# Performance work log

Measured on AMD Instinct MI355X. Metric: run time of the kernel, lower is better.

## Reference

```python
import jax, jax.numpy as jnp
import numpy as np

N = 10000      # nodes
E = 320000     # edges
IN = 256       # in_dim == out_dim
H = 8          # heads
D = 32         # head_dim = in_dim // heads
CLAMP = 5.0
BN_EPS = 1e-5


def setup_inputs() -> dict:
    key = jax.random.key(0)
    ks = jax.random.split(key, 24)
    s = 0.05
    nrm = lambda k, shape, sc=s: (jax.random.normal(k, shape, jnp.float32) * sc)
    inp = {
        "x": nrm(ks[0], (N, IN), 1.0),
        "edge_attr": nrm(ks[1], (E, IN), 1.0),
        "log_deg": jax.random.uniform(ks[2], (N, 1), jnp.float32, 0.1, 3.0),
        "edge_index": jax.random.randint(ks[3], (2, E), 0, N, jnp.int32),
        # attention projections (stored [in, out]; x @ W + b)
        "Qw": nrm(ks[4], (IN, H * D)), "Qb": jnp.zeros((H * D,), jnp.float32),
        "Kw": nrm(ks[5], (IN, H * D)), "Kb": jnp.zeros((H * D,), jnp.float32),
        "Ew": nrm(ks[6], (IN, H * D * 2)), "Eb": jnp.zeros((H * D * 2,), jnp.float32),
        "Vw": nrm(ks[7], (IN, H * D)), "Vb": jnp.zeros((H * D,), jnp.float32),
        "Aw": nrm(ks[8], (D, H, 1)),
        "VeRow": nrm(ks[9], (D, H, D)),
        # layer params
        "deg_coef": nrm(ks[10], (1, H * D, 2)),
        "Now": nrm(ks[11], (H * D, IN)), "Nob": jnp.zeros((IN,), jnp.float32),
        "Eow": nrm(ks[12], (H * D, IN)), "Eob": jnp.zeros((IN,), jnp.float32),
        "bn1n_g": jnp.ones((IN,), jnp.float32), "bn1n_b": jnp.zeros((IN,), jnp.float32),
        "bn1e_g": jnp.ones((IN,), jnp.float32), "bn1e_b": jnp.zeros((IN,), jnp.float32),
        "f1w": nrm(ks[13], (IN, 2 * IN)), "f1b": jnp.zeros((2 * IN,), jnp.float32),
        "f2w": nrm(ks[14], (2 * IN, IN)), "f2b": jnp.zeros((IN,), jnp.float32),
        "bn2_g": jnp.ones((IN,), jnp.float32), "bn2_b": jnp.zeros((IN,), jnp.float32),
    }
    return inp


def _bn(x, g, b):
    # batch_norm with batch statistics (bn_no_runner=True => track_running_stats=False)
    mu = jnp.mean(x, axis=0)
    var = jnp.mean(jnp.square(x - mu), axis=0)  # biased, as torch BN
    return (x - mu) * jax.lax.rsqrt(var + BN_EPS) * g + b


def _attention(x, edge_attr, edge_index, Qw, Qb, Kw, Kb, Ew, Eb, Vw, Vb, Aw, VeRow):
    n = x.shape[0]
    src, dst = edge_index[0], edge_index[1]
    Qh = (x @ Qw + Qb).reshape(n, H, D)
    Kh = (x @ Kw + Kb).reshape(n, H, D)
    Vh = (x @ Vw + Vb).reshape(n, H, D)
    Ex = (edge_attr @ Ew + Eb).reshape(-1, H, 2 * D)
    score1 = Kh[src] + Qh[dst]                      # [E,H,D]
    s2 = Ex[:, :, :D] * Ex[:, :, D:]
    score2 = jnp.sign(s2) * jnp.sqrt(jnp.abs(s2))   # == sqrt(relu(s2)) - sqrt(relu(-s2))
    conn = jax.nn.relu(score1 + score2)             # [E,H,D] (attn act='relu')
    score = jnp.einsum('ehd,dhc->ehc', conn, Aw)    # [E,H,1]
    score = jnp.clip(score, -CLAMP, CLAMP)
    # segment softmax over destination nodes
    m = jax.ops.segment_max(score, dst, num_segments=n)
    e = jnp.exp(score - m[dst])
    ssum = jax.ops.segment_sum(e, dst, num_segments=n)
    attn = e / (ssum[dst] + 1e-16)                  # [E,H,1]
    msg = Vh[src] * attn
    Vo = Qh + jax.ops.segment_sum(msg, dst, num_segments=n)
    rowV = jax.ops.segment_sum(conn * attn, dst, num_segments=n)
    rowV = jnp.einsum('nhd,dhc->nhc', rowV, VeRow)
    Vo = Vo + rowV
    return Vo.reshape(n, H * D), conn.reshape(-1, H * D)


def reference(x, edge_attr, log_deg, edge_index, Qw, Qb, Kw, Kb, Ew, Eb, Vw, Vb,
              Aw, VeRow, deg_coef, Now, Nob, Eow, Eob, bn1n_g, bn1n_b,
              bn1e_g, bn1e_b, f1w, f1b, f2w, f2b, bn2_g, bn2_b):
    nh, eh = _attention(x, edge_attr, edge_index, Qw, Qb, Kw, Kb, Ew, Eb, Vw, Vb, Aw, VeRow)
    # degree scaler
    nh = nh * deg_coef[:, :, 0] + (nh * log_deg) * deg_coef[:, :, 1]
    nh = nh @ Now + Nob
    eh = eh @ Eow + Eob
    nh = x + nh
    eh = edge_attr + eh
    nh = _bn(nh, bn1n_g, bn1n_b)
    eh = _bn(eh, bn1e_g, bn1e_b)
    ffn = jax.nn.relu(nh @ f1w + f1b) @ f2w + f2b
    nh = _bn(nh + ffn, bn2_g, bn2_b)
    return nh, eh
```

## Files before the change

kernel.cpp:

```cpp
#include <hip/hip_runtime.h>

#define NN 10000
#define NE 320000

typedef float f4 __attribute__((ext_vector_type(4)));
typedef float f32x4 __attribute__((ext_vector_type(4)));
typedef short bf16x8 __attribute__((ext_vector_type(8)));

__device__ __forceinline__ unsigned short f2b(float f) {
  unsigned u = __float_as_uint(f);
  u += 0x7fff + ((u >> 16) & 1);
  return (unsigned short)(u >> 16);
}
__device__ __forceinline__ float b2f(unsigned short s) {
  return __uint_as_float(((unsigned)s) << 16);
}
__device__ __forceinline__ bf16x8 pack8(f4 a, f4 b) {
  bf16x8 r;
  r[0] = (short)f2b(a[0]); r[1] = (short)f2b(a[1]);
  r[2] = (short)f2b(a[2]); r[3] = (short)f2b(a[3]);
  r[4] = (short)f2b(b[0]); r[5] = (short)f2b(b[1]);
  r[6] = (short)f2b(b[2]); r[7] = (short)f2b(b[3]);
  return r;
}
__device__ __forceinline__ int swz(int row, int k) {
  return (row * 256) + (k ^ ((row & 7) << 3));
}

__global__ void castw_k(const float* __restrict__ in, unsigned short* __restrict__ out,
                        int K, int lg)
{
  int idx = blockIdx.x * 256 + threadIdx.x;
  if (idx >= (K << lg)) return;
  int n = idx & ((1 << lg) - 1), k = idx >> lg;
  out[(size_t)n * K + k] = f2b(in[idx]);
}

__global__ void castb_k(const float* __restrict__ in, unsigned short* __restrict__ out,
                        long n8)
{
  long i = (long)blockIdx.x * 256 + threadIdx.x;
  if (i >= n8) return;
  const f4* p = (const f4*)(in + i * 8);
  *(bf16x8*)(out + i * 8) = pack8(p[0], p[1]);
}

__global__ void cat3_k(const float* __restrict__ a, const float* __restrict__ b,
                       const float* __restrict__ c, float* __restrict__ o)
{
  int t = threadIdx.x;
  o[t] = a[t]; o[256 + t] = b[t]; o[512 + t] = c[t];
}

__global__ __launch_bounds__(256) void gemm_bf16_k(
    const float* __restrict__ A, const unsigned short* __restrict__ BT,
    const float* __restrict__ bias, const float* __restrict__ res,
    float* __restrict__ C, float* __restrict__ stats,
    int M, int K, int NT, int flags)
{
  __shared__ unsigned short Al[64][40];
  __shared__ unsigned short Bl[128][40];
  const int t = threadIdx.x;
  const int n0 = blockIdx.x * 128;
  const int m0 = blockIdx.y * 64;
  const int lane = t & 63, c = lane & 15, g = lane >> 4, w = t >> 6;
  f32x4 acc[8] = {};
  for (int k0 = 0; k0 < K; k0 += 32) {
    {
      int row = t >> 2, kk = (t & 3) * 8;
      f4 v0 = {0.f,0.f,0.f,0.f}, v1 = {0.f,0.f,0.f,0.f};
      if (m0 + row < M) {
        const f4* p = (const f4*)(A + (size_t)(m0 + row) * K + k0 + kk);
        v0 = p[0]; v1 = p[1];
      }
      __syncthreads();
      *(bf16x8*)&Al[row][kk] = pack8(v0, v1);
    }
    {
      int col = t >> 1, kk = (t & 1) * 16;
      const bf16x8* p = (const bf16x8*)(BT + (size_t)(n0 + col) * K + k0 + kk);
      *(bf16x8*)&Bl[col][kk] = p[0];
      *(bf16x8*)&Bl[col][kk + 8] = p[1];
    }
    __syncthreads();
    bf16x8 a = *(bf16x8*)&Al[w * 16 + c][g * 8];
#pragma unroll
    for (int nb = 0; nb < 8; nb++) {
      bf16x8 b = *(bf16x8*)&Bl[nb * 16 + c][g * 8];
      acc[nb] = __builtin_amdgcn_mfma_f32_16x16x32_bf16(a, b, acc[nb], 0, 0, 0);
    }
  }
  const int do_relu = flags & 1, do_stats = flags & 2;
#pragma unroll
  for (int nb = 0; nb < 8; nb++) {
    const int col = n0 + nb * 16 + c;
    const float bs = bias[col];
    float sn = 0.f, qn = 0.f;
#pragma unroll
    for (int r = 0; r < 4; r++) {
      int row = m0 + w * 16 + g * 4 + r;
      if (row < M) {
        float v = acc[nb][r] + bs;
        if (res) v += res[(size_t)row * NT + col];
        if (do_relu) v = fmaxf(v, 0.f);
        C[(size_t)row * NT + col] = v;
        sn += v; qn += v * v;
      }
    }
    if (do_stats) {
      sn += __shfl_xor(sn, 16); sn += __shfl_xor(sn, 32);
      qn += __shfl_xor(qn, 16); qn += __shfl_xor(qn, 32);
      if (g == 0) {
        atomicAdd(&stats[col], sn);
        atomicAdd(&stats[NT + col], qn);
      }
    }
  }
}

__global__ __launch_bounds__(256) void edge_conn_k(
    const float* __restrict__ EA, const unsigned short* __restrict__ EwT,
    const float* __restrict__ Eb, const unsigned short* __restrict__ QKVb,
    const int* __restrict__ ei, const float* __restrict__ Aw,
    float* __restrict__ connf, unsigned short* __restrict__ connb,
    float* __restrict__ score, int CB)
{
  __shared__ unsigned short Abuf[16384];
  __shared__ unsigned short Bbuf[16384];
  float* Exl = (float*)Bbuf;
  const int t = threadIdx.x;
  const int e0 = blockIdx.x * 64;
  const int lane = t & 63, c = lane & 15, g = lane >> 4, w = t >> 6;
#pragma unroll
  for (int it = 0; it < 8; it++) {
    int o = t + it * 256;
    int row = o >> 5, kk = (o & 31) * 8;
    const f4* p = (const f4*)(EA + (size_t)(e0 + row) * 256 + kk);
    f4 v0 = p[0], v1 = p[1];
    *(bf16x8*)&Abuf[swz(row, kk)] = pack8(v0, v1);
  }
  const int m2 = t >> 2, dg = t & 3;
  const int e = e0 + m2;
  const int src = ei[e], dst = ei[NE + e];
  for (int h = 0; h < 8; h++) {
    __syncthreads();
#pragma unroll
    for (int it = 0; it < 8; it++) {
      int o = t + it * 256;
      int row = o >> 5, kk = (o & 31) * 8;
      *(bf16x8*)&Bbuf[swz(row, kk)] =
          *(const bf16x8*)(EwT + (size_t)(h * 64 + row) * 256 + kk);
    }
    __syncthreads();
    f32x4 acc[4] = {};
#pragma unroll
    for (int ks = 0; ks < 8; ks++) {
      bf16x8 a = *(bf16x8*)&Abuf[swz(w * 16 + c, ks * 32 + g * 8)];
#pragma unroll
      for (int cb = 0; cb < 4; cb++) {
        bf16x8 b = *(bf16x8*)&Bbuf[swz(cb * 16 + c, ks * 32 + g * 8)];
        acc[cb] = __builtin_amdgcn_mfma_f32_16x16x32_bf16(a, b, acc[cb], 0, 0, 0);
      }
    }
    __syncthreads();
#pragma unroll
    for (int cb = 0; cb < 4; cb++) {
      float eb = Eb[h * 64 + cb * 16 + c];
#pragma unroll
      for (int r = 0; r < 4; r++)
        Exl[(w * 16 + g * 4 + r) * 68 + cb * 16 + c] = acc[cb][r] + eb;
    }
    __syncthreads();
    const int cb2 = h * 32 + dg * 8;
    const float* ex = Exl + m2 * 68;
    f4 x1a = *(const f4*)(ex + dg * 8);
    f4 x1b = *(const f4*)(ex + dg * 8 + 4);
    f4 x2a = *(const f4*)(ex + 32 + dg * 8);
    f4 x2b = *(const f4*)(ex + 32 + dg * 8 + 4);
    bf16x8 kv8 = *(const bf16x8*)(QKVb + (size_t)src * 768 + 256 + cb2);
    bf16x8 qv8 = *(const bf16x8*)(QKVb + (size_t)dst * 768 + cb2);
    f4 c1, c2;
    float part = 0.f;
#pragma unroll
    for (int j = 0; j < 4; j++) {
      float s2 = x1a[j] * x2a[j];
      float v = copysignf(sqrtf(fabsf(s2)), s2)
              + b2f((unsigned short)kv8[j]) + b2f((unsigned short)qv8[j]);
      v = fmaxf(v, 0.f);
      c1[j] = v;
      part += v * Aw[(dg * 8 + j) * 8 + h];
      float s2b = x1b[j] * x2b[j];
      float vb = copysignf(sqrtf(fabsf(s2b)), s2b)
               + b2f((unsigned short)kv8[j + 4]) + b2f((unsigned short)qv8[j + 4]);
      vb = fmaxf(vb, 0.f);
      c2[j] = vb;
      part += vb * Aw[(dg * 8 + 4 + j) * 8 + h];
    }
    if (CB) {
      *(bf16x8*)(connb + (size_t)e * 256 + cb2) = pack8(c1, c2);
    } else {
      *(f4*)(connf + (size_t)e * 256 + cb2) = c1;
      *(f4*)(connf + (size_t)e * 256 + cb2 + 4) = c2;
    }
    part += __shfl_xor(part, 1);
    part += __shfl_xor(part, 2);
    if (dg == 0) score[(size_t)e * 8 + h] = fminf(fmaxf(part, -5.f), 5.f);
  }
}

__global__ void hist_k(const int* __restrict__ ei, int* __restrict__ cnt)
{
  int e = blockIdx.x * 256 + threadIdx.x;
  if (e < NE) atomicAdd(&cnt[ei[NE + e]], 1);
}

__global__ __launch_bounds__(256) void scan_k(const int* __restrict__ cnt, int* __restrict__ off)
{
  __shared__ int part[256];
  const int t = threadIdx.x;
  const int PER = 40;
  const int base = t * PER;
  int s = 0;
  for (int i = 0; i < PER; i++) {
    int b = base + i;
    if (b < NN) s += cnt[b];
  }
  part[t] = s;
  __syncthreads();
  for (int d = 1; d < 256; d <<= 1) {
    int v = (t >= d) ? part[t - d] : 0;
    __syncthreads();
    part[t] += v;
    __syncthreads();
  }
  int run = (t == 0) ? 0 : part[t - 1];
  for (int i = 0; i < PER; i++) {
    int b = base + i;
    if (b < NN) { off[b] = run; run += cnt[b]; }
  }
  if (t == 255) off[NN] = run;
}

__global__ void scat_k(const int* __restrict__ ei, const int* __restrict__ off,
                       int* __restrict__ cur, int* __restrict__ elist,
                       int* __restrict__ src_s)
{
  int e = blockIdx.x * 256 + threadIdx.x;
  if (e < NE) {
    int s = ei[e], d = ei[NE + e];
    int p = atomicAdd(&cur[d], 1);
    int j = off[d] + p;
    elist[j] = e;
    src_s[j] = s;
  }
}

__global__ __launch_bounds__(256) void node_agg_k(
    const int* __restrict__ off, const int* __restrict__ elist,
    const int* __restrict__ src_s, const float* __restrict__ score,
    const float* __restrict__ QKVh, const unsigned short* __restrict__ QKVb,
    const float* __restrict__ connf, const unsigned short* __restrict__ connb, int CB,
    const float* __restrict__ VeRow, const float* __restrict__ deg_coef,
    const float* __restrict__ log_deg, float* __restrict__ nh_a)
{
  const int n = blockIdx.x, t = threadIdx.x;
  const int h = t >> 5;
  __shared__ int eL[128];
  __shared__ int srcL[128];
  __shared__ float sS[1024];
  __shared__ float mS[8];
  __shared__ float rA[256];
  const int start = off[n];
  const int deg = off[n + 1] - start;
  float m = -1e30f, ssum = 0.f, vo = 0.f, ro = 0.f;
  for (int c0 = 0; c0 < deg; c0 += 128) {
    const int cn = min(128, deg - c0);
    __syncthreads();
    if (t < cn) {
      int jj = start + c0 + t;
      eL[t] = elist[jj];
      srcL[t] = src_s[jj];
    }
    __syncthreads();
    for (int i = t; i < cn * 8; i += 256) sS[i] = score[(size_t)eL[i >> 3] * 8 + (i & 7)];
    __syncthreads();
    float mc = -1e30f;
    for (int i = (t & 31); i < cn; i += 32) mc = fmaxf(mc, sS[i * 8 + h]);
    mc = fmaxf(mc, __shfl_xor(mc, 1));
    mc = fmaxf(mc, __shfl_xor(mc, 2));
    mc = fmaxf(mc, __shfl_xor(mc, 4));
    mc = fmaxf(mc, __shfl_xor(mc, 8));
    mc = fmaxf(mc, __shfl_xor(mc, 16));
    float nm = fmaxf(m, mc);
    if ((t & 31) == 0) mS[h] = nm;
    __syncthreads();
    for (int i = t; i < cn * 8; i += 256) sS[i] = __expf(sS[i] - mS[i & 7]);
    __syncthreads();
    float sc = __expf(m - nm);
    ssum *= sc; vo *= sc; ro *= sc;
    m = nm;
    int i = 0;
    if (CB) {
      for (; i + 4 <= cn; i += 4) {
        float w0 = sS[(i + 0) * 8 + h], w1 = sS[(i + 1) * 8 + h];
        float w2 = sS[(i + 2) * 8 + h], w3 = sS[(i + 3) * 8 + h];
        int s0 = srcL[i], s1 = srcL[i + 1], s2 = srcL[i + 2], s3 = srcL[i + 3];
        int f0 = eL[i], f1 = eL[i + 1], f2 = eL[i + 2], f3 = eL[i + 3];
        ssum += w0 + w1 + w2 + w3;
        vo = fmaf(w0, b2f(QKVb[(size_t)s0 * 768 + 512 + t]), vo);
        vo = fmaf(w1, b2f(QKVb[(size_t)s1 * 768 + 512 + t]), vo);
        vo = fmaf(w2, b2f(QKVb[(size_t)s2 * 768 + 512 + t]), vo);
        vo = fmaf(w3, b2f(QKVb[(size_t)s3 * 768 + 512 + t]), vo);
        ro = fmaf(w0, b2f(connb[(size_t)f0 * 256 + t]), ro);
        ro = fmaf(w1, b2f(connb[(size_t)f1 * 256 + t]), ro);
        ro = fmaf(w2, b2f(connb[(size_t)f2 * 256 + t]), ro);
        ro = fmaf(w3, b2f(connb[(size_t)f3 * 256 + t]), ro);
      }
      for (; i < cn; i++) {
        float w0 = sS[i * 8 + h];
        ssum += w0;
        vo = fmaf(w0, b2f(QKVb[(size_t)srcL[i] * 768 + 512 + t]), vo);
        ro = fmaf(w0, b2f(connb[(size_t)eL[i] * 256 + t]), ro);
      }
    } else {
      for (; i + 4 <= cn; i += 4) {
        float w0 = sS[(i + 0) * 8 + h], w1 = sS[(i + 1) * 8 + h];
        float w2 = sS[(i + 2) * 8 + h], w3 = sS[(i + 3) * 8 + h];
        int s0 = srcL[i], s1 = srcL[i + 1], s2 = srcL[i + 2], s3 = srcL[i + 3];
        int f0 = eL[i], f1 = eL[i + 1], f2 = eL[i + 2], f3 = eL[i + 3];
        ssum += w0 + w1 + w2 + w3;
        vo = fmaf(w0, QKVh[(size_t)s0 * 768 + 512 + t], vo);
        vo = fmaf(w1, QKVh[(size_t)s1 * 768 + 512 + t], vo);
        vo = fmaf(w2, QKVh[(size_t)s2 * 768 + 512 + t], vo);
        vo = fmaf(w3, QKVh[(size_t)s3 * 768 + 512 + t], vo);
        ro = fmaf(w0, connf[(size_t)f0 * 256 + t], ro);
        ro = fmaf(w1, connf[(size_t)f1 * 256 + t], ro);
        ro = fmaf(w2, connf[(size_t)f2 * 256 + t], ro);
        ro = fmaf(w3, connf[(size_t)f3 * 256 + t], ro);
      }
      for (; i < cn; i++) {
        float w0 = sS[i * 8 + h];
        ssum += w0;
        vo = fmaf(w0, QKVh[(size_t)srcL[i] * 768 + 512 + t], vo);
        ro = fmaf(w0, connf[(size_t)eL[i] * 256 + t], ro);
      }
    }
  }
  const float inv = 1.f / (ssum + 1e-16f);
  vo *= inv;
  ro *= inv;
  __syncthreads();
  rA[t] = ro;
  __syncthreads();
  float acc = 0.f;
#pragma unroll
  for (int d = 0; d < 32; d++) acc = fmaf(rA[h * 32 + d], VeRow[d * 256 + t], acc);
  float v = QKVh[(size_t)n * 768 + t] + vo + acc;
  const float ld = log_deg[n];
  v = v * (deg_coef[2 * t] + ld * deg_coef[2 * t + 1]);
  nh_a[(size_t)n * 256 + t] = v;
}

__global__ __launch_bounds__(256) void eh_gemm2_k(
    const unsigned short* __restrict__ EowT, const float* __restrict__ Eob,
    const float* __restrict__ EA, const unsigned short* __restrict__ connb,
    float* __restrict__ eh, float* __restrict__ stb)
{
  __shared__ unsigned short Al[64][40];
  __shared__ unsigned short Bl[256][40];
  __shared__ float lsum[256], lsq[256];
  const int t = threadIdx.x;
  const int e0 = blockIdx.x * 64;
  const int lane = t & 63, c = lane & 15, g = lane >> 4, w = t >> 6;
  lsum[t] = 0.f; lsq[t] = 0.f;
  f32x4 acc[16] = {};
  for (int ks = 0; ks < 8; ks++) {
    __syncthreads();
    {
      int row = t >> 2, kk = (t & 3) * 8;
      *(bf16x8*)&Al[row][kk] =
          *(const bf16x8*)(connb + (size_t)(e0 + row) * 256 + ks * 32 + kk);
    }
#pragma unroll
    for (int it = 0; it < 4; it++) {
      int o = t + it * 256;
      int row = o >> 2, kk = (o & 3) * 8;
      *(bf16x8*)&Bl[row][kk] = *(const bf16x8*)(EowT + (size_t)row * 256 + ks * 32 + kk);
    }
    __syncthreads();
    bf16x8 a = *(bf16x8*)&Al[w * 16 + c][g * 8];
#pragma unroll
    for (int nb = 0; nb < 16; nb++) {
      bf16x8 b = *(bf16x8*)&Bl[nb * 16 + c][g * 8];
      acc[nb] = __builtin_amdgcn_mfma_f32_16x16x32_bf16(a, b, acc[nb], 0, 0, 0);
    }
  }
#pragma unroll
  for (int nb = 0; nb < 16; nb++) {
    const int col = nb * 16 + c;
    const float eob = Eob[col];
    float sn = 0.f, qn = 0.f;
#pragma unroll
    for (int r = 0; r < 4; r++) {
      size_t row = e0 + w * 16 + g * 4 + r;
      float v = acc[nb][r] + eob + EA[row * 256 + col];
      eh[row * 256 + col] = v;
      sn += v; qn += v * v;
    }
    sn += __shfl_xor(sn, 16); sn += __shfl_xor(sn, 32);
    qn += __shfl_xor(qn, 16); qn += __shfl_xor(qn, 32);
    if (g == 0) { atomicAdd(&lsum[col], sn); atomicAdd(&lsq[col], qn); }
  }
  __syncthreads();
  float* dstb = stb + (size_t)(blockIdx.x & 63) * 512;
  atomicAdd(&dstb[t], lsum[t]);
  atomicAdd(&dstb[256 + t], lsq[t]);
}

__global__ __launch_bounds__(256) void eh_gemm_k(
    const unsigned short* __restrict__ EowT, const float* __restrict__ Eob,
    const float* __restrict__ EA, float* __restrict__ eh, float* __restrict__ stb)
{
  __shared__ unsigned short Al[64][264];
  __shared__ unsigned short Bl[256][40];
  __shared__ float lsum[256], lsq[256];
  const int t = threadIdx.x;
  const int e0 = blockIdx.x * 64;
  const int lane = t & 63, c = lane & 15, g = lane >> 4, w = t >> 6;
  lsum[t] = 0.f; lsq[t] = 0.f;
#pragma unroll
  for (int it = 0; it < 8; it++) {
    int o = t + it * 256;
    int row = o >> 5, kk = (o & 31) * 8;
    const f4* p = (const f4*)(eh + (size_t)(e0 + row) * 256 + kk);
    f4 v0 = p[0], v1 = p[1];
    *(bf16x8*)&Al[row][kk] = pack8(v0, v1);
  }
  f32x4 acc[16] = {};
  for (int ks = 0; ks < 8; ks++) {
    __syncthreads();
#pragma unroll
    for (int it = 0; it < 4; it++) {
      int o = t + it * 256;
      int row = o >> 2, kk = (o & 3) * 8;
      *(bf16x8*)&Bl[row][kk] = *(const bf16x8*)(EowT + (size_t)row * 256 + ks * 32 + kk);
    }
    __syncthreads();
    bf16x8 a = *(bf16x8*)&Al[w * 16 + c][ks * 32 + g * 8];
#pragma unroll
    for (int nb = 0; nb < 16; nb++) {
      bf16x8 b = *(bf16x8*)&Bl[nb * 16 + c][g * 8];
      acc[nb] = __builtin_amdgcn_mfma_f32_16x16x32_bf16(a, b, acc[nb], 0, 0, 0);
    }
  }
#pragma unroll
  for (int nb = 0; nb < 16; nb++) {
    const int col = nb * 16 + c;
    const float eob = Eob[col];
    float sn = 0.f, qn = 0.f;
#pragma unroll
    for (int r = 0; r < 4; r++) {
      size_t row = e0 + w * 16 + g * 4 + r;
      float v = acc[nb][r] + eob + EA[row * 256 + col];
      eh[row * 256 + col] = v;
      sn += v; qn += v * v;
    }
    sn += __shfl_xor(sn, 16); sn += __shfl_xor(sn, 32);
    qn += __shfl_xor(qn, 16); qn += __shfl_xor(qn, 32);
    if (g == 0) { atomicAdd(&lsum[col], sn); atomicAdd(&lsq[col], qn); }
  }
  __syncthreads();
  float* dstb = stb + (size_t)(blockIdx.x & 63) * 512;
  atomicAdd(&dstb[t], lsum[t]);
  atomicAdd(&dstb[256 + t], lsq[t]);
}

__global__ void bn_fin_k(float* __restrict__ st, float invR)
{
  int t = threadIdx.x;
  float mean = st[t] * invR;
  float var = st[256 + t] * invR - mean * mean;
  st[t] = mean;
  st[256 + t] = rsqrtf(var + 1e-5f);
}

__global__ void bn_fin_banked_k(const float* __restrict__ banks, float* __restrict__ st,
                                float invR)
{
  int t = threadIdx.x;
  float s = 0.f, q = 0.f;
  for (int b = 0; b < 64; b++) {
    s += banks[(size_t)b * 512 + t];
    q += banks[(size_t)b * 512 + 256 + t];
  }
  float mean = s * invR;
  float var = q * invR - mean * mean;
  st[t] = mean;
  st[256 + t] = rsqrtf(var + 1e-5f);
}

__global__ void bn_apply_k(const float* __restrict__ X, float* __restrict__ Y,
                           const float* __restrict__ st, const float* __restrict__ g,
                           const float* __restrict__ b, long nvec)
{
  long i = (long)blockIdx.x * 256 + threadIdx.x;
  if (i >= nvec) return;
  int base = (int)(i & 63) * 4;
  f4 x = *(const f4*)(X + i * 4);
  f4 mn = *(const f4*)(st + base);
  f4 rs = *(const f4*)(st + 256 + base);
  f4 gg = *(const f4*)(g + base);
  f4 bb = *(const f4*)(b + base);
  f4 y;
#pragma unroll
  for (int j = 0; j < 4; j++) y[j] = (x[j] - mn[j]) * rs[j] * gg[j] + bb[j];
  *(f4*)(Y + i * 4) = y;
}

extern "C" void kernel_launch(void* const* d_in, const int* in_sizes, int n_in,
                              void* d_out, int out_size, void* d_ws, size_t ws_size,
                              hipStream_t stream)
{
  (void)in_sizes; (void)n_in; (void)out_size;
  const float* x        = (const float*)d_in[0];
  const float* edge_attr= (const float*)d_in[1];
  const float* log_deg  = (const float*)d_in[2];
  const int*   ei       = (const int*)d_in[3];
  const float* Qw = (const float*)d_in[4];  const float* Qb = (const float*)d_in[5];
  const float* Kw = (const float*)d_in[6];  const float* Kb = (const float*)d_in[7];
  const float* Ew = (const float*)d_in[8];  const float* Eb = (const float*)d_in[9];
  const float* Vw = (const float*)d_in[10]; const float* Vb = (const float*)d_in[11];
  const float* Aw = (const float*)d_in[12]; const float* VeRow = (const float*)d_in[13];
  const float* deg_coef = (const float*)d_in[14];
  const float* Now = (const float*)d_in[15]; const float* Nob = (const float*)d_in[16];
  const float* Eow = (const float*)d_in[17]; const float* Eob = (const float*)d_in[18];
  const float* bn1n_g = (const float*)d_in[19]; const float* bn1n_b = (const float*)d_in[20];
  const float* bn1e_g = (const float*)d_in[21]; const float* bn1e_b = (const float*)d_in[22];
  const float* f1w = (const float*)d_in[23]; const float* f1b = (const float*)d_in[24];
  const float* f2w = (const float*)d_in[25]; const float* f2b = (const float*)d_in[26];
  const float* bn2_g = (const float*)d_in[27]; const float* bn2_b = (const float*)d_in[28];

  float* out_nh = (float*)d_out;
  float* out_eh = out_nh + (size_t)NN * 256;

  float* ws     = (float*)d_ws;
  float* QKVh   = ws;
  unsigned short* QKVb = (unsigned short*)(QKVh + (size_t)NN * 768);
  float* score  = (float*)(QKVb + (size_t)NN * 768);
  float* nh_a   = score + 2560000;
  float* nh2    = nh_a + 2560000;
  float* ffn1   = nh2 + 2560000;
  float* st1    = ffn1 + 5120000;
  float* st2    = st1 + 512;
  float* st3    = st2 + 512;
  float* stb    = st3 + 512;
  float* biasQKV= stb + 64 * 512;
  unsigned short* QwT = (unsigned short*)(biasQKV + 768);
  unsigned short* KwT = QwT + 65536;
  unsigned short* VwT = KwT + 65536;
  unsigned short* NowT= VwT + 65536;
  unsigned short* EowT= NowT + 65536;
  unsigned short* EwT = EowT + 65536;
  unsigned short* f1wT= EwT + 131072;
  unsigned short* f2wT= f1wT + 131072;
  int*   cnt    = (int*)(f2wT + 131072);
  int*   off    = cnt + NN;
  int*   cur    = off + NN + 1;
  int*   elist  = cur + NN;
  int*   src_s  = elist + NE;
  unsigned short* connb = (unsigned short*)(src_s + NE);
  size_t need = (size_t)((char*)(connb + (size_t)NE * 256) - (char*)d_ws);
  const int CB = (ws_size >= need) ? 1 : 0;

  hipMemsetAsync(cnt, 0, (size_t)NN * 4, stream);
  hipMemsetAsync(cur, 0, (size_t)NN * 4, stream);
  hipMemsetAsync(st1, 0, (size_t)2 * 512 * 4, stream);
  hipMemsetAsync(stb, 0, (size_t)64 * 512 * 4, stream);

  dim3 blk(256);

  castw_k<<<dim3(256), blk, 0, stream>>>(Qw, QwT, 256, 8);
  castw_k<<<dim3(256), blk, 0, stream>>>(Kw, KwT, 256, 8);
  castw_k<<<dim3(256), blk, 0, stream>>>(Vw, VwT, 256, 8);
  castw_k<<<dim3(256), blk, 0, stream>>>(Now, NowT, 256, 8);
  castw_k<<<dim3(256), blk, 0, stream>>>(Eow, EowT, 256, 8);
  castw_k<<<dim3(512), blk, 0, stream>>>(Ew, EwT, 256, 9);
  castw_k<<<dim3(512), blk, 0, stream>>>(f1w, f1wT, 256, 9);
  castw_k<<<dim3(512), blk, 0, stream>>>(f2w, f2wT, 512, 8);
  cat3_k<<<dim3(1), blk, 0, stream>>>(Qb, Kb, Vb, biasQKV);

  hist_k<<<dim3(NE / 256), blk, 0, stream>>>(ei, cnt);
  scan_k<<<dim3(1), blk, 0, stream>>>(cnt, off);
  scat_k<<<dim3(NE / 256), blk, 0, stream>>>(ei, off, cur, elist, src_s);

  gemm_bf16_k<<<dim3(6, 157), blk, 0, stream>>>(x, QwT, biasQKV, nullptr, QKVh, nullptr,
                                                NN, 256, 768, 0);
  castb_k<<<dim3((NN * 96 + 255) / 256), blk, 0, stream>>>(QKVh, QKVb, (long)NN * 96);

  edge_conn_k<<<dim3(NE / 64), blk, 0, stream>>>(edge_attr, EwT, Eb, QKVb, ei, Aw,
                                                 out_eh, connb, score, CB);

  node_agg_k<<<dim3(NN), blk, 0, stream>>>(off, elist, src_s, score, QKVh, QKVb,
                                           out_eh, connb, CB,
                                           VeRow, deg_coef, log_deg, nh_a);

  if (CB) {
    eh_gemm2_k<<<dim3(NE / 64), blk, 0, stream>>>(EowT, Eob, edge_attr, connb,
                                                  out_eh, stb);
  } else {
    eh_gemm_k<<<dim3(NE / 64), blk, 0, stream>>>(EowT, Eob, edge_attr, out_eh, stb);
  }
  bn_fin_banked_k<<<dim3(1), blk, 0, stream>>>(stb, st3, 1.0f / NE);
  bn_apply_k<<<dim3(NE * 64 / 256), blk, 0, stream>>>(out_eh, out_eh, st3,
                                                      bn1e_g, bn1e_b, (long)NE * 64);

  gemm_bf16_k<<<dim3(2, 157), blk, 0, stream>>>(nh_a, NowT, Nob, x, out_nh, st1,
                                                NN, 256, 256, 2);
  bn_fin_k<<<dim3(1), blk, 0, stream>>>(st1, 1.0f / NN);
  bn_apply_k<<<dim3(NN * 64 / 256), blk, 0, stream>>>(out_nh, nh2, st1,
                                                      bn1n_g, bn1n_b, (long)NN * 64);
  gemm_bf16_k<<<dim3(4, 157), blk, 0, stream>>>(nh2, f1wT, f1b, nullptr, ffn1, nullptr,
                                                NN, 256, 512, 1);
  gemm_bf16_k<<<dim3(2, 157), blk, 0, stream>>>(ffn1, f2wT, f2b, nh2, out_nh, st2,
                                                NN, 512, 256, 2);
  bn_fin_k<<<dim3(1), blk, 0, stream>>>(st2, 1.0f / NN);
  bn_apply_k<<<dim3(NN * 64 / 256), blk, 0, stream>>>(out_nh, out_nh, st2,
                                                      bn2_g, bn2_b, (long)NN * 64);
}
```

Baseline: 991.0 us.

## Shrink edge_conn LDS footprint, keep A fragments in registers, drop barriers

The edge-attribute A fragments are loaded once into registers, so the A and B tiles can share one LDS buffer. The edge projection scratch is stored as bf16 in a smaller padded buffer. Each wave reads back only its own rows, which lets two per-head barriers go, and the K/Q gathers are issued at the start of each head iteration. Launch bounds now request 3 blocks per SM to raise occupancy. In exchange, register pressure rises and rounding the intermediate edge projection to bf16 adds a small precision loss.

Measured after the change: 951.0 us. 4.0% less time.

```diff
diff --git a/kernel.cpp b/kernel.cpp
--- a/kernel.cpp
+++ b/kernel.cpp
@@ -118,16 +118,15 @@
   }
 }
 
-__global__ __launch_bounds__(256) void edge_conn_k(
+__global__ __launch_bounds__(256, 3) void edge_conn_k(
     const float* __restrict__ EA, const unsigned short* __restrict__ EwT,
     const float* __restrict__ Eb, const unsigned short* __restrict__ QKVb,
     const int* __restrict__ ei, const float* __restrict__ Aw,
     float* __restrict__ connf, unsigned short* __restrict__ connb,
     float* __restrict__ score, int CB)
 {
-  __shared__ unsigned short Abuf[16384];
-  __shared__ unsigned short Bbuf[16384];
-  float* Exl = (float*)Bbuf;
+  __shared__ unsigned short sh[16384];
+  __shared__ unsigned short ExlB[64 * 72];
   const int t = threadIdx.x;
   const int e0 = blockIdx.x * 64;
   const int lane = t & 63, c = lane & 15, g = lane >> 4, w = t >> 6;
@@ -137,74 +136,84 @@
     int row = o >> 5, kk = (o & 31) * 8;
     const f4* p = (const f4*)(EA + (size_t)(e0 + row) * 256 + kk);
     f4 v0 = p[0], v1 = p[1];
-    *(bf16x8*)&Abuf[swz(row, kk)] = pack8(v0, v1);
+    *(bf16x8*)&sh[swz(row, kk)] = pack8(v0, v1);
   }
   const int m2 = t >> 2, dg = t & 3;
   const int e = e0 + m2;
   const int src = ei[e], dst = ei[NE + e];
+  const unsigned short* kbase = QKVb + (size_t)src * 768 + 256 + dg * 8;
+  const unsigned short* qbase = QKVb + (size_t)dst * 768 + dg * 8;
+  __syncthreads();
+  bf16x8 areg[8];
+#pragma unroll
+  for (int i = 0; i < 8; i++)
+    areg[i] = *(bf16x8*)&sh[swz(w * 16 + c, i * 32 + g * 8)];
+  __syncthreads();
+
   for (int h = 0; h < 8; h++) {
-    __syncthreads();
+    bf16x8 kv8 = *(const bf16x8*)(kbase + h * 32);
+    bf16x8 qv8 = *(const bf16x8*)(qbase + h * 32);
 #pragma unroll
     for (int it = 0; it < 8; it++) {
       int o = t + it * 256;
       int row = o >> 5, kk = (o & 31) * 8;
-      *(bf16x8*)&Bbuf[swz(row, kk)] =
+      *(bf16x8*)&sh[swz(row, kk)] =
           *(const bf16x8*)(EwT + (size_t)(h * 64 + row) * 256 + kk);
     }
     __syncthreads();
     f32x4 acc[4] = {};
 #pragma unroll
     for (int ks = 0; ks < 8; ks++) {
-      bf16x8 a = *(bf16x8*)&Abuf[swz(w * 16 + c, ks * 32 + g * 8)];
+      bf16x8 a = areg[ks];
 #pragma unroll
       for (int cb = 0; cb < 4; cb++) {
-        bf16x8 b = *(bf16x8*)&Bbuf[swz(cb * 16 + c, ks * 32 + g * 8)];
+        bf16x8 b = *(bf16x8*)&sh[swz(cb * 16 + c, ks * 32 + g * 8)];
         acc[cb] = __builtin_amdgcn_mfma_f32_16x16x32_bf16(a, b, acc[cb], 0, 0, 0);
       }
     }
-    __syncthreads();
 #pragma unroll
     for (int cb = 0; cb < 4; cb++) {
       float eb = Eb[h * 64 + cb * 16 + c];
 #pragma unroll
       for (int r = 0; r < 4; r++)
-        Exl[(w * 16 + g * 4 + r) * 68 + cb * 16 + c] = acc[cb][r] + eb;
-    }
-    __syncthreads();
-    const int cb2 = h * 32 + dg * 8;
-    const float* ex = Exl + m2 * 68;
-    f4 x1a = *(const f4*)(ex + dg * 8);
-    f4 x1b = *(const f4*)(ex + dg * 8 + 4);
-    f4 x2a = *(const f4*)(ex + 32 + dg * 8);
-    f4 x2b = *(const f4*)(ex + 32 + dg * 8 + 4);
-    bf16x8 kv8 = *(const bf16x8*)(QKVb + (size_t)src * 768 + 256 + cb2);
-    bf16x8 qv8 = *(const bf16x8*)(QKVb + (size_t)dst * 768 + cb2);
-    f4 c1, c2;
-    float part = 0.f;
-#pragma unroll
-    for (int j = 0; j < 4; j++) {
-      float s2 = x1a[j] * x2a[j];
-      float v = copysignf(sqrtf(fabsf(s2)), s2)
-              + b2f((unsigned short)kv8[j]) + b2f((unsigned short)qv8[j]);
-      v = fmaxf(v, 0.f);
-      c1[j] = v;
-      part += v * Aw[(dg * 8 + j) * 8 + h];
-      float s2b = x1b[j] * x2b[j];
-      float vb = copysignf(sqrtf(fabsf(s2b)), s2b)
-               + b2f((unsigned short)kv8[j + 4]) + b2f((unsigned short)qv8[j + 4]);
-      vb = fmaxf(vb, 0.f);
-      c2[j] = vb;
-      part += vb * Aw[(dg * 8 + 4 + j) * 8 + h];
-    }
-    if (CB) {
-      *(bf16x8*)(connb + (size_t)e * 256 + cb2) = pack8(c1, c2);
-    } else {
-      *(f4*)(connf + (size_t)e * 256 + cb2) = c1;
-      *(f4*)(connf + (size_t)e * 256 + cb2 + 4) = c2;
-    }
-    part += __shfl_xor(part, 1);
-    part += __shfl_xor(part, 2);
-    if (dg == 0) score[(size_t)e * 8 + h] = fminf(fmaxf(part, -5.f), 5.f);
+        ExlB[(w * 16 + g * 4 + r) * 72 + cb * 16 + c] = f2b(acc[cb][r] + eb);
+    }
+    {
+      bf16x8 x1 = *(bf16x8*)&ExlB[m2 * 72 + dg * 8];
+      bf16x8 x2 = *(bf16x8*)&ExlB[m2 * 72 + 32 + dg * 8];
+      const int cb2 = h * 32 + dg * 8;
+      f4 c1, c2;
+      float part = 0.f;
+#pragma unroll
+      for (int j = 0; j < 4; j++) {
+        float ex1 = b2f((unsigned short)x1[j]);
+        float ex2 = b2f((unsigned short)x2[j]);
+        float s2 = ex1 * ex2;
+        float v = copysignf(sqrtf(fabsf(s2)), s2)
+                + b2f((unsigned short)kv8[j]) + b2f((unsigned short)qv8[j]);
+        v = fmaxf(v, 0.f);
+        c1[j] = v;
+        part += v * Aw[(dg * 8 + j) * 8 + h];
+        float ex1b = b2f((unsigned short)x1[j + 4]);
+        float ex2b = b2f((unsigned short)x2[j + 4]);
+        float s2b = ex1b * ex2b;
+        float vb = copysignf(sqrtf(fabsf(s2b)), s2b)
+                 + b2f((unsigned short)kv8[j + 4]) + b2f((unsigned short)qv8[j + 4]);
+        vb = fmaxf(vb, 0.f);
+        c2[j] = vb;
+        part += vb * Aw[(dg * 8 + 4 + j) * 8 + h];
+      }
+      if (CB) {
+        *(bf16x8*)(connb + (size_t)e * 256 + cb2) = pack8(c1, c2);
+      } else {
+        *(f4*)(connf + (size_t)e * 256 + cb2) = c1;
+        *(f4*)(connf + (size_t)e * 256 + cb2 + 4) = c2;
+      }
+      part += __shfl_xor(part, 1);
+      part += __shfl_xor(part, 2);
+      if (dg == 0) score[(size_t)e * 8 + h] = fminf(fmaxf(part, -5.f), 5.f);
+    }
+    __syncthreads();
   }
 }
 
```
